# Kernel tuning notes

Measured on AMD Instinct MI355X. Metric: run time of the kernel, lower is better.

## Reference

```python
import jax, jax.numpy as jnp
import numpy as np

ALPHA = 1.0
BETA = 10.0
MARGIN = 0.5


def setup_inputs() -> dict:
    key = jax.random.key(0)
    k1, k2 = jax.random.split(key)
    emb = jax.random.normal(k1, (4096, 512), dtype=jnp.float32)
    # module docstring: embeddings are L2-normalized
    emb = emb / jnp.linalg.norm(emb, axis=1, keepdims=True)
    labels = jax.random.randint(k2, (4096,), 0, 64, dtype=jnp.int64)
    return {"embeddings": emb, "labels": labels}


def reference(embeddings, labels):
    n = embeddings.shape[0]
    sim = embeddings @ embeddings.T  # [n, n]
    labels_eq = labels[None, :] == labels[:, None]
    eye = jnp.eye(n, dtype=bool)
    pos_mask = labels_eq & ~eye
    neg_mask = ~labels_eq & ~eye

    # masked exp-sums (masked entries contribute 0, matching torch's
    # clone/NEG_INF/zero-out dance without materializing extra copies)
    pos_exp = jnp.where(pos_mask, jnp.exp(-ALPHA * (sim - MARGIN)), 0.0)
    neg_exp = jnp.where(neg_mask, jnp.exp(BETA * (sim - MARGIN)), 0.0)
    pos_term = (1.0 / ALPHA) * jnp.log1p(pos_exp.sum(axis=1))
    neg_term = (1.0 / BETA) * jnp.log1p(neg_exp.sum(axis=1))

    valid = pos_mask.any(axis=1) & neg_mask.any(axis=1)
    n_valid = valid.sum()
    total = jnp.where(valid, pos_term + neg_term, 0.0).sum()
    return jnp.where(n_valid > 0, total / jnp.maximum(n_valid, 1).astype(sim.dtype), 0.0)
```

## Files before the change

kernel.cpp:

```cpp
#include <hip/hip_runtime.h>
#include <hip/hip_bf16.h>

#define N 4096
#define D 512
#define MARGIN 0.5f
#define BETA 10.0f

typedef __attribute__((ext_vector_type(8))) short short8;
typedef __attribute__((ext_vector_type(4))) float floatx4;

__device__ inline unsigned short f2bf(float f) {
    unsigned u = __float_as_uint(f);
    u += 0x7fffu + ((u >> 16) & 1u);
    return (unsigned short)(u >> 16);
}

__global__ __launch_bounds__(256) void convert_bf16_kernel(
        const float4* __restrict__ in, ushort4* __restrict__ out,
        float* __restrict__ sums ) {
    int idx = blockIdx.x * 256 + threadIdx.x;
    if (idx < 2 * N) sums[idx] = 0.f;
    float4 v = in[idx];
    ushort4 o;
    o.x = f2bf(v.x); o.y = f2bf(v.y); o.z = f2bf(v.z); o.w = f2bf(v.w);
    out[idx] = o;
}

__global__ __launch_bounds__(256, 4) void ms_loss_gemm(
        const unsigned short* __restrict__ Ebf,
        const int* __restrict__ labels,
        float* __restrict__ pos_sum,
        float* __restrict__ neg_sum) {
    __shared__ unsigned short Atile[2][128 * 32];
    __shared__ unsigned short Btile[2][128 * 32];
    __shared__ int rlab[128];
    __shared__ int clab[128];

    int t = blockIdx.x;
    int bi = 0;
    while (t >= (32 - bi)) { t -= (32 - bi); ++bi; }
    const int bj = bi + t;
    const bool diag = (bi == bj);

    const int tid  = threadIdx.x;
    const int wave = tid >> 6;
    const int lane = tid & 63;
    const int quad = lane >> 4;
    const int lcol = lane & 15;
    const int wrow = wave >> 1;
    const int wcol = wave & 1;
    const int ibase = bi * 128;
    const int jbase = bj * 128;

    if (tid < 128)       rlab[tid]       = labels[ibase + tid];
    else                 clab[tid - 128] = labels[jbase + tid - 128];

    floatx4 acc[4][4];
#pragma unroll
    for (int mt = 0; mt < 4; ++mt)
#pragma unroll
        for (int nt = 0; nt < 4; ++nt)
            acc[mt][nt] = (floatx4){0.f, 0.f, 0.f, 0.f};

    const char* Eb = (const char*)Ebf;
    char* Ab = (char*)Atile;
    char* Bb = (char*)Btile;
    const int srow = lane >> 2;
    const int sckb = ((lane & 3) ^ ((lane >> 3) & 3)) * 16;
    const int rdsw = ((lcol >> 1) & 3);

#define STAGE(BUF, KT)                                                         \
    do {                                                                       \
        const int kb_ = (KT) * 64;                                             \
        _Pragma("unroll")                                                      \
        for (int it_ = 0; it_ < 2; ++it_) {                                    \
            int r_    = wave * 16 + it_ * 64 + srow;                           \
            int ldso_ = (BUF) * 8192 + wave * 1024 + it_ * 4096 + lane * 16;   \
            const char* ga_ = Eb + (size_t)(ibase + r_) * (D * 2) + kb_ + sckb;\
            __builtin_amdgcn_global_load_lds(                                  \
                (const __attribute__((address_space(1))) void*)ga_,            \
                (__attribute__((address_space(3))) void*)(Ab + ldso_), 16, 0, 0);\
            if (!diag) {                                                       \
                const char* gb_ = Eb + (size_t)(jbase + r_) * (D * 2) + kb_ + sckb;\
                __builtin_amdgcn_global_load_lds(                              \
                    (const __attribute__((address_space(1))) void*)gb_,        \
                    (__attribute__((address_space(3))) void*)(Bb + ldso_), 16, 0, 0);\
            }                                                                  \
        }                                                                      \
    } while (0)

    STAGE(0, 0);
    __syncthreads();

#pragma unroll 2
    for (int kt = 0; kt < D / 32; ++kt) {
        const int cur = kt & 1;
        if (kt < D / 32 - 1) STAGE(cur ^ 1, kt + 1);

        const char* Ar = Ab + cur * 8192;
        const char* Br = diag ? Ar : (Bb + cur * 8192);

        short8 a[4], b[4];
        const int rchunk = (quad ^ rdsw) * 16;
#pragma unroll
        for (int mt = 0; mt < 4; ++mt) {
            int r = wrow * 64 + mt * 16 + lcol;
            a[mt] = *(const short8*)(Ar + r * 64 + rchunk);
        }
#pragma unroll
        for (int nt = 0; nt < 4; ++nt) {
            int c = wcol * 64 + nt * 16 + lcol;
            b[nt] = *(const short8*)(Br + c * 64 + rchunk);
        }
#pragma unroll
        for (int mt = 0; mt < 4; ++mt)
#pragma unroll
            for (int nt = 0; nt < 4; ++nt)
                acc[mt][nt] = __builtin_amdgcn_mfma_f32_16x16x32_bf16(
                    a[mt], b[nt], acc[mt][nt], 0, 0, 0);

        __syncthreads();
    }
#undef STAGE

    int ljv[4], gjv[4];
#pragma unroll
    for (int nt = 0; nt < 4; ++nt) {
        int cl = wcol * 64 + nt * 16 + lcol;
        ljv[nt] = clab[cl];
        gjv[nt] = jbase + cl;
    }

    float colp[4] = {0.f, 0.f, 0.f, 0.f};
    float coln[4] = {0.f, 0.f, 0.f, 0.f};

#pragma unroll
    for (int mt = 0; mt < 4; ++mt) {
#pragma unroll
        for (int reg = 0; reg < 4; ++reg) {
            int rl = wrow * 64 + mt * 16 + quad * 4 + reg;
            int gi = ibase + rl;
            int li = rlab[rl];
            float p = 0.f, ng = 0.f;
#pragma unroll
            for (int nt = 0; nt < 4; ++nt) {
                float s = acc[mt][nt][reg];
                if (gi != gjv[nt]) {
                    if (li == ljv[nt]) {
                        float e = __expf(MARGIN - s);
                        p += e;  colp[nt] += e;
                    } else {
                        float e = __expf(BETA * (s - MARGIN));
                        ng += e; coln[nt] += e;
                    }
                }
            }
            p  += __shfl_xor(p, 1);   ng += __shfl_xor(ng, 1);
            p  += __shfl_xor(p, 2);   ng += __shfl_xor(ng, 2);
            p  += __shfl_xor(p, 4);   ng += __shfl_xor(ng, 4);
            p  += __shfl_xor(p, 8);   ng += __shfl_xor(ng, 8);
            if (lcol == 0) {
                atomicAdd(&pos_sum[gi], p);
                atomicAdd(&neg_sum[gi], ng);
            }
        }
    }

    if (!diag) {
#pragma unroll
        for (int nt = 0; nt < 4; ++nt) {
            float cp = colp[nt], cn = coln[nt];
            cp += __shfl_xor(cp, 16);  cn += __shfl_xor(cn, 16);
            cp += __shfl_xor(cp, 32);  cn += __shfl_xor(cn, 32);
            if (quad == 0) {
                int gj = gjv[nt];
                atomicAdd(&pos_sum[gj], cp);
                atomicAdd(&neg_sum[gj], cn);
            }
        }
    }
}

__global__ __launch_bounds__(1024) void finalize_kernel(
        const float4* __restrict__ pos4, const float4* __restrict__ neg4,
        float* __restrict__ out) {
    __shared__ float sb[16];
    __shared__ int   sc[16];
    const int tid = threadIdx.x;
    float4 p  = pos4[tid];
    float4 ng = neg4[tid];
    const float* pp = (const float*)&p;
    const float* nn = (const float*)&ng;
    float tot = 0.f;
    int cnt = 0;
#pragma unroll
    for (int j = 0; j < 4; ++j) {
        if (pp[j] > 0.f && nn[j] > 0.f) {
            tot += log1pf(pp[j]) + (1.0f / BETA) * log1pf(nn[j]);
            cnt += 1;
        }
    }
#pragma unroll
    for (int s = 1; s < 64; s <<= 1) {
        tot += __shfl_xor(tot, s);
        cnt += __shfl_xor(cnt, s);
    }
    if ((tid & 63) == 0) { sb[tid >> 6] = tot; sc[tid >> 6] = cnt; }
    __syncthreads();
    if (tid < 16) {
        float t2 = sb[tid];
        int   c2 = sc[tid];
#pragma unroll
        for (int s = 1; s < 16; s <<= 1) {
            t2 += __shfl_xor(t2, s);
            c2 += __shfl_xor(c2, s);
        }
        if (tid == 0) out[0] = (c2 > 0) ? t2 / (float)c2 : 0.f;
    }
}

extern "C" void kernel_launch(void* const* d_in, const int* in_sizes, int n_in,
                              void* d_out, int out_size, void* d_ws, size_t ws_size,
                              hipStream_t stream) {
    const float* emb   = (const float*)d_in[0];
    const int* labels  = (const int*)d_in[1];
    float* out         = (float*)d_out;

    char* ws = (char*)d_ws;
    unsigned short* Ebf = (unsigned short*)ws;
    float* pos_sum = (float*)(ws + (size_t)N * D * 2);
    float* neg_sum = pos_sum + N;

    convert_bf16_kernel<<<(N * D / 4) / 256, 256, 0, stream>>>(
        (const float4*)emb, (ushort4*)Ebf, pos_sum);

    ms_loss_gemm<<<(32 * 33) / 2, 256, 0, stream>>>(Ebf, labels, pos_sum, neg_sum);

    finalize_kernel<<<1, 1024, 0, stream>>>(
        (const float4*)pos_sum, (const float4*)neg_sum, out);
}
```

Baseline: 88.85 us.

## Fuse finalize into GEMM via last-block ticket and use fine-grained waitcnt pipelining

Removes the separate finalize kernel launch. A global ticket counter now lets the last finishing GEMM block compute the final loss, and the convert kernel zeros the ticket. The k-loop drops __syncthreads in favor of explicit vmcnt/lgkmcnt waits and raw barriers, so the next stage's loads can stay in flight across the barrier. Diagonal tiles now also load the B tile, which adds redundant traffic but removes a branch. The explicit waitcnt reasoning risks correctness if the outstanding-load counts are wrong.

```diff
diff --git a/kernel.cpp b/kernel.cpp
--- a/kernel.cpp
+++ b/kernel.cpp
@@ -5,6 +5,8 @@
 #define D 512
 #define MARGIN 0.5f
 #define BETA 10.0f
+#define NT (D / 32)
+#define NBLOCKS 528
 
 typedef __attribute__((ext_vector_type(8))) short short8;
 typedef __attribute__((ext_vector_type(4))) float floatx4;
@@ -19,7 +21,7 @@
         const float4* __restrict__ in, ushort4* __restrict__ out,
         float* __restrict__ sums ) {
     int idx = blockIdx.x * 256 + threadIdx.x;
-    if (idx < 2 * N) sums[idx] = 0.f;
+    if (idx <= 2 * N) sums[idx] = 0.f;
     float4 v = in[idx];
     ushort4 o;
     o.x = f2bf(v.x); o.y = f2bf(v.y); o.z = f2bf(v.z); o.w = f2bf(v.w);
@@ -30,11 +32,16 @@
         const unsigned short* __restrict__ Ebf,
         const int* __restrict__ labels,
         float* __restrict__ pos_sum,
-        float* __restrict__ neg_sum) {
+        float* __restrict__ neg_sum,
+        unsigned* __restrict__ ticket,
+        float* __restrict__ out) {
     __shared__ unsigned short Atile[2][128 * 32];
     __shared__ unsigned short Btile[2][128 * 32];
     __shared__ int rlab[128];
     __shared__ int clab[128];
+    __shared__ int is_last;
+    __shared__ float fb[4];
+    __shared__ int   fc[4];
 
     int t = blockIdx.x;
     int bi = 0;
@@ -80,48 +87,56 @@
             __builtin_amdgcn_global_load_lds(                                  \
                 (const __attribute__((address_space(1))) void*)ga_,            \
                 (__attribute__((address_space(3))) void*)(Ab + ldso_), 16, 0, 0);\
-            if (!diag) {                                                       \
-                const char* gb_ = Eb + (size_t)(jbase + r_) * (D * 2) + kb_ + sckb;\
-                __builtin_amdgcn_global_load_lds(                              \
-                    (const __attribute__((address_space(1))) void*)gb_,        \
-                    (__attribute__((address_space(3))) void*)(Bb + ldso_), 16, 0, 0);\
-            }                                                                  \
+            const char* gb_ = Eb + (size_t)(jbase + r_) * (D * 2) + kb_ + sckb;\
+            __builtin_amdgcn_global_load_lds(                                  \
+                (const __attribute__((address_space(1))) void*)gb_,            \
+                (__attribute__((address_space(3))) void*)(Bb + ldso_), 16, 0, 0);\
         }                                                                      \
     } while (0)
 
+#define COMPUTE(CUR)                                                           \
+    do {                                                                       \
+        const char* Ar = Ab + (CUR) * 8192;                                    \
+        const char* Br = Bb + (CUR) * 8192;                                    \
+        short8 a[4], b[4];                                                     \
+        const int rchunk = (quad ^ rdsw) * 16;                                 \
+        _Pragma("unroll")                                                      \
+        for (int mt = 0; mt < 4; ++mt) {                                       \
+            int r = wrow * 64 + mt * 16 + lcol;                                \
+            a[mt] = *(const short8*)(Ar + r * 64 + rchunk);                    \
+        }                                                                      \
+        _Pragma("unroll")                                                      \
+        for (int nt = 0; nt < 4; ++nt) {                                       \
+            int c = wcol * 64 + nt * 16 + lcol;                                \
+            b[nt] = *(const short8*)(Br + c * 64 + rchunk);                    \
+        }                                                                      \
+        _Pragma("unroll")                                                      \
+        for (int mt = 0; mt < 4; ++mt)                                         \
+            _Pragma("unroll")                                                  \
+            for (int nt = 0; nt < 4; ++nt)                                     \
+                acc[mt][nt] = __builtin_amdgcn_mfma_f32_16x16x32_bf16(         \
+                    a[mt], b[nt], acc[mt][nt], 0, 0, 0);                       \
+    } while (0)
+
     STAGE(0, 0);
-    __syncthreads();
-
-#pragma unroll 2
-    for (int kt = 0; kt < D / 32; ++kt) {
-        const int cur = kt & 1;
-        if (kt < D / 32 - 1) STAGE(cur ^ 1, kt + 1);
-
-        const char* Ar = Ab + cur * 8192;
-        const char* Br = diag ? Ar : (Bb + cur * 8192);
-
-        short8 a[4], b[4];
-        const int rchunk = (quad ^ rdsw) * 16;
-#pragma unroll
-        for (int mt = 0; mt < 4; ++mt) {
-            int r = wrow * 64 + mt * 16 + lcol;
-            a[mt] = *(const short8*)(Ar + r * 64 + rchunk);
-        }
-#pragma unroll
-        for (int nt = 0; nt < 4; ++nt) {
-            int c = wcol * 64 + nt * 16 + lcol;
-            b[nt] = *(const short8*)(Br + c * 64 + rchunk);
-        }
-#pragma unroll
-        for (int mt = 0; mt < 4; ++mt)
-#pragma unroll
-            for (int nt = 0; nt < 4; ++nt)
-                acc[mt][nt] = __builtin_amdgcn_mfma_f32_16x16x32_bf16(
-                    a[mt], b[nt], acc[mt][nt], 0, 0, 0);
-
-        __syncthreads();
-    }
+
+    for (int kt = 0; kt < NT - 1; ++kt) {
+        STAGE((kt + 1) & 1, kt + 1);
+        asm volatile("s_waitcnt vmcnt(4)" ::: "memory");
+        __builtin_amdgcn_s_barrier();
+        asm volatile("" ::: "memory");
+        COMPUTE(kt & 1);
+        asm volatile("s_waitcnt lgkmcnt(0)" ::: "memory");
+        __builtin_amdgcn_s_barrier();
+        asm volatile("" ::: "memory");
+    }
+    asm volatile("s_waitcnt vmcnt(0)" ::: "memory");
+    __builtin_amdgcn_s_barrier();
+    asm volatile("" ::: "memory");
+    COMPUTE((NT - 1) & 1);
+
 #undef STAGE
+#undef COMPUTE
 
     int ljv[4], gjv[4];
 #pragma unroll
@@ -179,43 +194,46 @@
             }
         }
     }
-}
-
-__global__ __launch_bounds__(1024) void finalize_kernel(
-        const float4* __restrict__ pos4, const float4* __restrict__ neg4,
-        float* __restrict__ out) {
-    __shared__ float sb[16];
-    __shared__ int   sc[16];
-    const int tid = threadIdx.x;
-    float4 p  = pos4[tid];
-    float4 ng = neg4[tid];
-    const float* pp = (const float*)&p;
-    const float* nn = (const float*)&ng;
-    float tot = 0.f;
-    int cnt = 0;
-#pragma unroll
-    for (int j = 0; j < 4; ++j) {
-        if (pp[j] > 0.f && nn[j] > 0.f) {
-            tot += log1pf(pp[j]) + (1.0f / BETA) * log1pf(nn[j]);
-            cnt += 1;
-        }
-    }
-#pragma unroll
-    for (int s = 1; s < 64; s <<= 1) {
-        tot += __shfl_xor(tot, s);
-        cnt += __shfl_xor(cnt, s);
-    }
-    if ((tid & 63) == 0) { sb[tid >> 6] = tot; sc[tid >> 6] = cnt; }
+
+    __threadfence();
+    if (tid == 0) {
+        unsigned old = atomicAdd(ticket, 1u);
+        is_last = (old == NBLOCKS - 1);
+    }
     __syncthreads();
-    if (tid < 16) {
-        float t2 = sb[tid];
-        int   c2 = sc[tid];
-#pragma unroll
-        for (int s = 1; s < 16; s <<= 1) {
-            t2 += __shfl_xor(t2, s);
-            c2 += __shfl_xor(c2, s);
-        }
-        if (tid == 0) out[0] = (c2 > 0) ? t2 / (float)c2 : 0.f;
+    if (is_last) {
+        __threadfence();
+        const float4* pos4 = (const float4*)pos_sum;
+        const float4* neg4 = (const float4*)neg_sum;
+        float tot = 0.f;
+        int cnt = 0;
+#pragma unroll
+        for (int k = 0; k < 4; ++k) {
+            int i = k * 256 + tid;
+            float4 p  = pos4[i];
+            float4 ng = neg4[i];
+            const float* pp = (const float*)&p;
+            const float* nn = (const float*)&ng;
+#pragma unroll
+            for (int j = 0; j < 4; ++j) {
+                if (pp[j] > 0.f && nn[j] > 0.f) {
+                    tot += log1pf(pp[j]) + (1.0f / BETA) * log1pf(nn[j]);
+                    cnt += 1;
+                }
+            }
+        }
+#pragma unroll
+        for (int s = 1; s < 64; s <<= 1) {
+            tot += __shfl_xor(tot, s);
+            cnt += __shfl_xor(cnt, s);
+        }
+        if (lane == 0) { fb[wave] = tot; fc[wave] = cnt; }
+        __syncthreads();
+        if (tid == 0) {
+            float T = fb[0] + fb[1] + fb[2] + fb[3];
+            int   C = fc[0] + fc[1] + fc[2] + fc[3];
+            out[0] = (C > 0) ? T / (float)C : 0.f;
+        }
     }
 }
 
@@ -230,12 +248,11 @@
     unsigned short* Ebf = (unsigned short*)ws;
     float* pos_sum = (float*)(ws + (size_t)N * D * 2);
     float* neg_sum = pos_sum + N;
+    unsigned* ticket = (unsigned*)(neg_sum + N);
 
     convert_bf16_kernel<<<(N * D / 4) / 256, 256, 0, stream>>>(
         (const float4*)emb, (ushort4*)Ebf, pos_sum);
 
-    ms_loss_gemm<<<(32 * 33) / 2, 256, 0, stream>>>(Ebf, labels, pos_sum, neg_sum);
-
-    finalize_kernel<<<1, 1024, 0, stream>>>(
-        (const float4*)pos_sum, (const float4*)neg_sum, out);
-}
+    ms_loss_gemm<<<NBLOCKS, 256, 0, stream>>>(
+        Ebf, labels, pos_sum, neg_sum, ticket, out);
+}
```

Measured after the change: 115.8 us. 1.3x slower.
